# Kernel optimization log

Measured on AMD Instinct MI355X. Metric: run time of the kernel, lower is better.

## Reference

```python
import jax, jax.numpy as jnp
import numpy as np

D_MODEL, N_HEADS, N_KV, D_K = 4096, 32, 8, 128
N_REP = N_HEADS // N_KV  # n_kv_groups
SEQ = 2048
EPS = 1e-6


def _layernorm(x, gamma, beta):
    # LayerNorm over the last (d_k) axis
    mu = jnp.mean(x, axis=-1, keepdims=True)
    var = jnp.var(x, axis=-1, keepdims=True)
    return (x - mu) * jax.lax.rsqrt(var + EPS) * gamma + beta


def setup_inputs() -> dict:
    key = jax.random.key(0)
    ks = jax.random.split(key, 8)
    s = 0.02
    return {
        "x": jax.random.normal(ks[0], (1, SEQ, D_MODEL), jnp.float32),
        "k_cache": jnp.zeros((N_KV, SEQ, D_K), jnp.float32),
        "v_cache": jnp.zeros((N_KV, SEQ, D_K), jnp.float32),
        "Wq": jax.random.normal(ks[1], (N_HEADS * D_K, D_MODEL), jnp.float32) * s,
        "Wk": jax.random.normal(ks[2], (N_KV * D_K, D_MODEL), jnp.float32) * s,
        "Wv": jax.random.normal(ks[3], (N_KV * D_K, D_MODEL), jnp.float32) * s,
        "Wo": jax.random.normal(ks[4], (D_MODEL, D_MODEL), jnp.float32) * s,
        "q_gamma": jnp.ones((D_K,), jnp.float32),
        "q_beta": jnp.zeros((D_K,), jnp.float32),
        "k_gamma": jnp.ones((D_K,), jnp.float32),
        "k_beta": jnp.zeros((D_K,), jnp.float32),
        "positions": jnp.arange(SEQ, dtype=jnp.int32),
        "seq_id": 0,
    }


def reference(x, k_cache, v_cache, Wq, Wk, Wv, Wo, q_gamma, q_beta, k_gamma, k_beta, positions, seq_id):
    B, S, _ = x.shape
    # projections (no bias: attention_bias=False)
    q = (x @ Wq.T).reshape(B, S, N_HEADS, D_K)
    k = (x @ Wk.T).reshape(B, S, N_KV, D_K)
    v = (x @ Wv.T).reshape(B, S, N_KV, D_K)
    # per-head LayerNorm on d_k (q_norm / k_norm)
    q = _layernorm(q, q_gamma, q_beta)
    k = _layernorm(k, k_gamma, k_beta)
    # rotary in the source is identity (SimpleRotary returns x unchanged)
    # paged-cache update: scatter new K/V (batch 0) into cache at `positions`
    k_cache = k_cache.at[:, positions, :].set(jnp.swapaxes(k[0], 0, 1))  # [n_kv, S, d_k]
    v_cache = v_cache.at[:, positions, :].set(jnp.swapaxes(v[0], 0, 1))
    # gather cached KV up to max position (prefill: full SEQ, static for jit)
    K = k_cache[None, :, :S, :]  # [1, n_kv, S, d_k]
    V = v_cache[None, :, :S, :]
    # GQA repeat_kv: expand kv heads to n_heads
    K = jnp.repeat(K, N_REP, axis=1)  # [1, n_heads, S, d_k]
    V = jnp.repeat(V, N_REP, axis=1)
    Q = jnp.swapaxes(q, 1, 2)  # [B, n_heads, S, d_k]
    # causal SDPA (dropout_p=0 in eval)
    scores = jnp.einsum("bhqd,bhkd->bhqk", Q, K) / jnp.sqrt(jnp.float32(D_K))
    causal = jnp.tril(jnp.ones((S, S), dtype=bool))
    scores = jnp.where(causal, scores, jnp.finfo(scores.dtype).min)
    attn = jax.nn.softmax(scores, axis=-1)
    out = jnp.einsum("bhqk,bhkd->bhqd", attn, V)  # [B, n_heads, S, d_k]
    out = jnp.swapaxes(out, 1, 2).reshape(B, S, D_MODEL)
    return out @ Wo.T
```

## Files before the change

kernel.cpp:

```cpp
#include <hip/hip_runtime.h>
#include <stdint.h>

typedef short bf16x8 __attribute__((ext_vector_type(8)));
typedef float f32x4 __attribute__((ext_vector_type(4)));
typedef float f32x16 __attribute__((ext_vector_type(16)));

#define SEQ     2048
#define DM      4096
#define NQH     32
#define NKVH    8
#define DK      128
#define NQKV    6144

__device__ __forceinline__ unsigned short f2bfb(float f) {
    union { float f; unsigned u; } x; x.f = f;
    unsigned r = x.u + 0x7FFFu + ((x.u >> 16) & 1u);
    return (unsigned short)(r >> 16);
}

__device__ __forceinline__ unsigned cvt_pk_bf16(float a, float b) {
    unsigned r;
    asm("v_cvt_pk_bf16_f32 %0, %1, %2" : "=v"(r) : "v"(a), "v"(b));
    return r;
}

#if __has_builtin(__builtin_amdgcn_exp2f)
__device__ __forceinline__ float exp2_fast(float x) { return __builtin_amdgcn_exp2f(x); }
#else
__device__ __forceinline__ float exp2_fast(float x) { return exp2f(x); }
#endif

__device__ __forceinline__ void stage16(const void* g, void* l) {
    __builtin_amdgcn_global_load_lds(
        (const __attribute__((address_space(1))) void*)g,
        (__attribute__((address_space(3))) void*)l,
        16, 0, 0);
}

__global__ __launch_bounds__(256)
void cvt_bf16(const float4* __restrict__ src, ushort4* __restrict__ dst, int n4) {
    int i = blockIdx.x * 256 + threadIdx.x;
    const int stride = gridDim.x * 256;
    for (; i < n4; i += stride) {
        float4 f = src[i];
        ushort4 u;
        u.x = f2bfb(f.x); u.y = f2bfb(f.y); u.z = f2bfb(f.z); u.w = f2bfb(f.w);
        dst[i] = u;
    }
}

__global__ __launch_bounds__(256, 2)
void gemm_bt(const unsigned short* __restrict__ A, const unsigned short* __restrict__ B,
             float* __restrict__ C, int M, int N, int K)
{
    __shared__ __align__(16) unsigned short As[128 * 32];
    __shared__ __align__(16) unsigned short Bs[128 * 32];

    const int tid = threadIdx.x;
    const int w  = tid >> 6;
    const int l  = tid & 63;
    const int lr = l & 15;
    const int lg = l >> 4;
    const int m0 = blockIdx.y << 7;
    const int n0 = blockIdx.x << 7;
    const int wm = (w >> 1) << 6;
    const int wn = (w & 1) << 6;

    f32x4 acc[4][4];
#pragma unroll
    for (int i = 0; i < 4; ++i)
#pragma unroll
        for (int j = 0; j < 4; ++j) acc[i][j] = f32x4{0.f, 0.f, 0.f, 0.f};

    const int c0   = tid;
    const int row0 = c0 >> 2, kc0 = (c0 & 3) << 3;
    const int c1   = tid + 256;
    const int row1 = c1 >> 2, kc1 = (c1 & 3) << 3;
    const unsigned short* Ag = A + (size_t)m0 * K;
    const unsigned short* Bg = B + (size_t)n0 * K;
    char* AsB = (char*)As;
    char* BsB = (char*)Bs;
    const int wb = w << 10;

    const int nk = K >> 5;
    for (int kt = 0; kt < nk; ++kt) {
        const int ko = kt << 5;
        stage16(Ag + (size_t)row0 * K + ko + kc0, AsB + wb);
        stage16(Ag + (size_t)row1 * K + ko + kc1, AsB + 4096 + wb);
        stage16(Bg + (size_t)row0 * K + ko + kc0, BsB + wb);
        stage16(Bg + (size_t)row1 * K + ko + kc1, BsB + 4096 + wb);
        __syncthreads();

        bf16x8 af[4], bfr[4];
#pragma unroll
        for (int mi = 0; mi < 4; ++mi)
            af[mi] = *(const bf16x8*)(As + ((wm + (mi << 4) + lr) << 5) + (lg << 3));
#pragma unroll
        for (int ni = 0; ni < 4; ++ni)
            bfr[ni] = *(const bf16x8*)(Bs + ((wn + (ni << 4) + lr) << 5) + (lg << 3));
#pragma unroll
        for (int mi = 0; mi < 4; ++mi)
#pragma unroll
            for (int ni = 0; ni < 4; ++ni)
                acc[mi][ni] = __builtin_amdgcn_mfma_f32_16x16x32_bf16(af[mi], bfr[ni], acc[mi][ni], 0, 0, 0);
        __syncthreads();
    }

#pragma unroll
    for (int mi = 0; mi < 4; ++mi)
#pragma unroll
        for (int ni = 0; ni < 4; ++ni) {
            const int row = m0 + wm + (mi << 4) + (lg << 2);
            const int col = n0 + wn + (ni << 4) + lr;
            float* cp = C + (size_t)row * N + col;
#pragma unroll
            for (int r = 0; r < 4; ++r) cp[(size_t)r * N] = acc[mi][ni][r];
        }
}

__global__ __launch_bounds__(256)
void ln_qk(const float* __restrict__ Y,
           const float* __restrict__ qg, const float* __restrict__ qb,
           const float* __restrict__ kg, const float* __restrict__ kb,
           unsigned short* __restrict__ Q, unsigned short* __restrict__ Kc)
{
    const int seg = blockIdx.x * 4 + (threadIdx.x >> 6);
    const int l = threadIdx.x & 63;
    const int s = seg / 40;
    const int hh = seg - s * 40;

    const float* y = Y + (size_t)s * NQKV + hh * 128;
    float2 v = *(const float2*)(y + l * 2);
    float sum = v.x + v.y;
    float sq  = v.x * v.x + v.y * v.y;
#pragma unroll
    for (int d = 1; d < 64; d <<= 1) {
        sum += __shfl_xor(sum, d);
        sq  += __shfl_xor(sq, d);
    }
    const float mu  = sum * (1.f / 128.f);
    const float var = sq * (1.f / 128.f) - mu * mu;
    const float rs  = rsqrtf(var + 1e-6f);

    const float* g = (hh < 32) ? qg : kg;
    const float* b = (hh < 32) ? qb : kb;
    const float c = (hh < 32) ? (0.08838834764831845f * 1.4426950408889634f) : 1.0f;
    const float g0 = g[l * 2], g1 = g[l * 2 + 1];
    const float b0 = b[l * 2], b1 = b[l * 2 + 1];
    const unsigned short o0 = f2bfb(((v.x - mu) * rs * g0 + b0) * c);
    const unsigned short o1 = f2bfb(((v.y - mu) * rs * g1 + b1) * c);
    const unsigned pack = (unsigned)o0 | ((unsigned)o1 << 16);

    if (hh < 32) {
        unsigned* dst = (unsigned*)(Q + ((size_t)hh * SEQ + s) * 128 + l * 2);
        *dst = pack;
    } else {
        unsigned* dst = (unsigned*)(Kc + ((size_t)(hh - 32) * SEQ + s) * 128 + l * 2);
        *dst = pack;
    }
}

__global__ __launch_bounds__(256)
void v_transpose(const float* __restrict__ Y, unsigned short* __restrict__ Vt)
{
    __shared__ unsigned short t[64][132];
    const int h  = blockIdx.x;
    const int s0 = blockIdx.y << 6;
    const int tid = threadIdx.x;
    const float* y = Y + (size_t)s0 * NQKV + 5120 + h * 128;

#pragma unroll
    for (int p = 0; p < 16; ++p) {
        const int idx = p * 512 + tid * 2;
        const int s = idx >> 7, d = idx & 127;
        float2 v = *(const float2*)(y + (size_t)s * NQKV + d);
        t[s][d]     = f2bfb(v.x);
        t[s][d + 1] = f2bfb(v.y);
    }
    __syncthreads();
    unsigned short* out = Vt + (size_t)h * 128 * SEQ + s0;
#pragma unroll
    for (int p = 0; p < 16; ++p) {
        const int idx = p * 512 + tid * 2;
        const int d = idx >> 6, sp = idx & 63;
        unsigned pack = (unsigned)t[sp][d] | ((unsigned)t[sp + 1][d] << 16);
        *(unsigned*)(out + (size_t)d * SEQ + sp) = pack;
    }
}

__global__ __launch_bounds__(256, 2)
void attn(const unsigned short* __restrict__ Qb, const unsigned short* __restrict__ Kb,
          const unsigned short* __restrict__ Vt, unsigned short* __restrict__ Ob)
{
    __shared__ __align__(16) unsigned short Kl[2][64 * 128];
    __shared__ __align__(16) unsigned short Vl[2][128 * 64];

    const int h   = blockIdx.x;
    const int qt  = 15 - blockIdx.y;
    const int kvh = h >> 2;
    const int tid = threadIdx.x;
    const int w   = tid >> 6;
    const int l   = tid & 63;
    const int lq  = l & 31;
    const int hi  = l >> 5;
    const int q0  = qt << 7;
    const int wq  = q0 + (w << 5);
    const int qrow = wq + lq;

    const unsigned short* Qh = Qb + ((size_t)h * SEQ + wq) * 128;
    const unsigned short* Kh = Kb + (size_t)kvh * SEQ * 128;
    const unsigned short* Vh = Vt + (size_t)kvh * 128 * SEQ;

    int koff[4], voff[4];
#pragma unroll
    for (int p = 0; p < 4; ++p) {
        const int c  = p * 256 + tid;
        const int kr = c >> 4, kc = c & 15;
        koff[p] = kr * 128 + ((kc ^ (kr & 7)) << 3);
        const int vr = c >> 3, vc = c & 7;
        voff[p] = vr * SEQ + ((vc ^ (vr & 7)) << 3);
    }
    const int dstb = w << 10;

    bf16x8 qf[8];
#pragma unroll
    for (int ks = 0; ks < 8; ++ks)
        qf[ks] = *(const bf16x8*)(Qh + lq * 128 + ks * 16 + hi * 8);

    f32x16 o0_ = {0}, o1_ = {0}, o2_ = {0}, o3_ = {0};
    float m = -1.0e30f, lsum = 0.f;

    const int nt = (q0 + 128) >> 6;
    const int sw = (lq & 7) << 4;

#pragma unroll
    for (int p = 0; p < 4; ++p)
        stage16(Kh + koff[p], (char*)Kl[0] + p * 4096 + dstb);
#pragma unroll
    for (int p = 0; p < 4; ++p)
        stage16(Vh + voff[p], (char*)Vl[0] + p * 4096 + dstb);
    __syncthreads();

    int buf = 0;
    for (int t = 0; t < nt; ++t) {
        const int kv0 = t << 6;

        if (t + 1 < nt) {
            const int kvn = kv0 + 64;
#pragma unroll
            for (int p = 0; p < 4; ++p)
                stage16(Kh + (size_t)kvn * 128 + koff[p], (char*)(Kl[buf ^ 1]) + p * 4096 + dstb);
#pragma unroll
            for (int p = 0; p < 4; ++p)
                stage16(Vh + kvn + voff[p], (char*)(Vl[buf ^ 1]) + p * 4096 + dstb);
        }

        if (kv0 <= wq + 31) {
            const char* Kb0 = (const char*)(Kl[buf]) + lq * 256;
            const char* Kb1 = (const char*)(Kl[buf]) + (lq + 32) * 256;
            bf16x8 kf0[8], kf1[8];
#pragma unroll
            for (int ks = 0; ks < 8; ++ks) {
                const int cb = (ks * 32 + hi * 16) ^ sw;
                kf0[ks] = *(const bf16x8*)(Kb0 + cb);
                kf1[ks] = *(const bf16x8*)(Kb1 + cb);
            }
            f32x16 s0 = {0}, s1 = {0};
            __builtin_amdgcn_s_setprio(1);
#pragma unroll
            for (int ks = 0; ks < 8; ++ks) {
                s0 = __builtin_amdgcn_mfma_f32_32x32x16_bf16(kf0[ks], qf[ks], s0, 0, 0, 0);
                s1 = __builtin_amdgcn_mfma_f32_32x32x16_bf16(kf1[ks], qf[ks], s1, 0, 0, 0);
            }
            __builtin_amdgcn_s_setprio(0);

            if (kv0 + 63 > wq) {
#pragma unroll
                for (int r = 0; r < 16; ++r) {
                    const int kvl = (r & 3) + 8 * (r >> 2) + 4 * hi;
                    if (kv0 + kvl > qrow)      s0[r] = -1.0e30f;
                    if (kv0 + 32 + kvl > qrow) s1[r] = -1.0e30f;
                }
            }

            float m8[8];
#pragma unroll
            for (int i = 0; i < 8; ++i)
                m8[i] = fmaxf(fmaxf(s0[i], s0[i + 8]), fmaxf(s1[i], s1[i + 8]));
#pragma unroll
            for (int i = 0; i < 4; ++i) m8[i] = fmaxf(m8[i], m8[i + 4]);
            float pm = fmaxf(fmaxf(m8[0], m8[1]), fmaxf(m8[2], m8[3]));
            pm = fmaxf(pm, __shfl_xor(pm, 32));

            if (!__all(pm - m <= 8.0f)) {
                const float mn = fmaxf(m, pm);
                const float al = exp2_fast(m - mn);
                lsum *= al;
#pragma unroll
                for (int r = 0; r < 16; ++r) { o0_[r] *= al; o1_[r] *= al; o2_[r] *= al; o3_[r] *= al; }
                m = mn;
            }

#pragma unroll
            for (int r = 0; r < 16; ++r) s0[r] = exp2_fast(s0[r] - m);
#pragma unroll
            for (int r = 0; r < 16; ++r) s1[r] = exp2_fast(s1[r] - m);
            float a8[8];
#pragma unroll
            for (int i = 0; i < 8; ++i)
                a8[i] = (s0[i] + s0[i + 8]) + (s1[i] + s1[i + 8]);
#pragma unroll
            for (int i = 0; i < 4; ++i) a8[i] += a8[i + 4];
            float rs = (a8[0] + a8[1]) + (a8[2] + a8[3]);
            rs += __shfl_xor(rs, 32);
            lsum += rs;

            unsigned pw0[2][4], pw1[2][4];
#pragma unroll
            for (int u = 0; u < 4; ++u) {
                pw0[0][u] = cvt_pk_bf16(s0[u * 4 + 0], s0[u * 4 + 1]);
                pw1[0][u] = cvt_pk_bf16(s0[u * 4 + 2], s0[u * 4 + 3]);
                pw0[1][u] = cvt_pk_bf16(s1[u * 4 + 0], s1[u * 4 + 1]);
                pw1[1][u] = cvt_pk_bf16(s1[u * 4 + 2], s1[u * 4 + 3]);
            }

            const char* Vb = (const char*)(Vl[buf]);
#pragma unroll
            for (int ksg = 0; ksg < 4; ++ksg) {
                const int b  = ksg >> 1;
                const int ks = ksg & 1;
                const unsigned a0 = pw0[b][2 * ks],     a1 = pw1[b][2 * ks];
                const unsigned b0 = pw0[b][2 * ks + 1], b1 = pw1[b][2 * ks + 1];
                const unsigned sa0 = __shfl_xor(a0, 32);
                const unsigned sb0 = __shfl_xor(b0, 32);
                const unsigned sa1 = __shfl_xor(a1, 32);
                const unsigned sb1 = __shfl_xor(b1, 32);
                union { unsigned wrd[4]; bf16x8 v; } pb;
                pb.wrd[0] = hi ? sb0 : a0;
                pb.wrd[1] = hi ? sb1 : a1;
                pb.wrd[2] = hi ? b0  : sa0;
                pb.wrd[3] = hi ? b1  : sa1;

                const int cb = (ksg * 32 + hi * 16) ^ sw;
                bf16x8 vf0 = *(const bf16x8*)(Vb + (lq)       * 128 + cb);
                bf16x8 vf1 = *(const bf16x8*)(Vb + (lq + 32)  * 128 + cb);
                bf16x8 vf2 = *(const bf16x8*)(Vb + (lq + 64)  * 128 + cb);
                bf16x8 vf3 = *(const bf16x8*)(Vb + (lq + 96)  * 128 + cb);
                __builtin_amdgcn_s_setprio(1);
                o0_ = __builtin_amdgcn_mfma_f32_32x32x16_bf16(vf0, pb.v, o0_, 0, 0, 0);
                o1_ = __builtin_amdgcn_mfma_f32_32x32x16_bf16(vf1, pb.v, o1_, 0, 0, 0);
                o2_ = __builtin_amdgcn_mfma_f32_32x32x16_bf16(vf2, pb.v, o2_, 0, 0, 0);
                o3_ = __builtin_amdgcn_mfma_f32_32x32x16_bf16(vf3, pb.v, o3_, 0, 0, 0);
                __builtin_amdgcn_s_setprio(0);
            }
        }

        __syncthreads();
        buf ^= 1;
    }

    const float inv = 1.0f / lsum;
    unsigned short* orow = Ob + (size_t)qrow * DM + h * 128;
#pragma unroll
    for (int r = 0; r < 16; r += 2) {
        const int doff = 8 * (r >> 2) + 4 * hi + (r & 3);
        *(unsigned*)(orow + 0  + doff) = cvt_pk_bf16(o0_[r] * inv, o0_[r + 1] * inv);
        *(unsigned*)(orow + 32 + doff) = cvt_pk_bf16(o1_[r] * inv, o1_[r + 1] * inv);
        *(unsigned*)(orow + 64 + doff) = cvt_pk_bf16(o2_[r] * inv, o2_[r + 1] * inv);
        *(unsigned*)(orow + 96 + doff) = cvt_pk_bf16(o3_[r] * inv, o3_[r + 1] * inv);
    }
}

extern "C" void kernel_launch(void* const* d_in, const int* in_sizes, int n_in,
                              void* d_out, int out_size, void* d_ws, size_t ws_size,
                              hipStream_t stream)
{
    const float* x  = (const float*)d_in[0];
    const float* Wq = (const float*)d_in[3];
    const float* Wk = (const float*)d_in[4];
    const float* Wv = (const float*)d_in[5];
    const float* Wo = (const float*)d_in[6];
    const float* qg = (const float*)d_in[7];
    const float* qb = (const float*)d_in[8];
    const float* kg = (const float*)d_in[9];
    const float* kb = (const float*)d_in[10];
    float* out = (float*)d_out;

    char* ws = (char*)d_ws;
    unsigned short* xb   = (unsigned short*)(ws);
    unsigned short* wqkv = (unsigned short*)(ws + 16777216);
    unsigned short* wo   = (unsigned short*)(ws + 67108864);
    float*          y    = (float*)        (ws + 100663296);
    unsigned short* qbuf = (unsigned short*)(ws + 150994944);
    unsigned short* kbuf = (unsigned short*)(ws + 167772160);
    unsigned short* vtb  = (unsigned short*)(ws + 171966464);
    unsigned short* ob   = (unsigned short*)(ws + 176160768);

    {
        int n4 = (SEQ * DM) / 4;
        cvt_bf16<<<2048, 256, 0, stream>>>((const float4*)x, (ushort4*)xb, n4);
        n4 = (NQH * DK * DM) / 4;
        cvt_bf16<<<2048, 256, 0, stream>>>((const float4*)Wq, (ushort4*)wqkv, n4);
        n4 = (NKVH * DK * DM) / 4;
        cvt_bf16<<<2048, 256, 0, stream>>>((const float4*)Wk, (ushort4*)(wqkv + 16777216), n4);
        cvt_bf16<<<2048, 256, 0, stream>>>((const float4*)Wv, (ushort4*)(wqkv + 20971520), n4);
        n4 = (DM * DM) / 4;
        cvt_bf16<<<2048, 256, 0, stream>>>((const float4*)Wo, (ushort4*)wo, n4);
    }

    gemm_bt<<<dim3(NQKV / 128, SEQ / 128), 256, 0, stream>>>(xb, wqkv, y, SEQ, NQKV, DM);

    ln_qk<<<(SEQ * 40) / 4, 256, 0, stream>>>(y, qg, qb, kg, kb, qbuf, kbuf);

    v_transpose<<<dim3(NKVH, SEQ / 64), 256, 0, stream>>>(y, vtb);

    attn<<<dim3(NQH, SEQ / 128), 256, 0, stream>>>(qbuf, kbuf, vtb, ob);

    gemm_bt<<<dim3(DM / 128, SEQ / 128), 256, 0, stream>>>(ob, wo, out, SEQ, DM, DM);
}
```

Baseline: 527.9 us.

## Rewrite GEMM with 256x128 tiles, double-buffered LDS, XOR swizzle, block remap

Result: slower. 588.0 us (+11.4%).

```diff
diff --git a/kernel.cpp b/kernel.cpp
--- a/kernel.cpp
+++ b/kernel.cpp
@@ -49,69 +49,125 @@
     }
 }
 
-__global__ __launch_bounds__(256, 2)
-void gemm_bt(const unsigned short* __restrict__ A, const unsigned short* __restrict__ B,
+__global__ __launch_bounds__(512, 2)
+void gemm256(const unsigned short* __restrict__ A, const unsigned short* __restrict__ B,
              float* __restrict__ C, int M, int N, int K)
 {
-    __shared__ __align__(16) unsigned short As[128 * 32];
-    __shared__ __align__(16) unsigned short Bs[128 * 32];
+    __shared__ __align__(16) char lds[2 * 49152];
 
     const int tid = threadIdx.x;
-    const int w  = tid >> 6;
-    const int l  = tid & 63;
-    const int lr = l & 15;
-    const int lg = l >> 4;
-    const int m0 = blockIdx.y << 7;
-    const int n0 = blockIdx.x << 7;
-    const int wm = (w >> 1) << 6;
-    const int wn = (w & 1) << 6;
-
-    f32x4 acc[4][4];
-#pragma unroll
-    for (int i = 0; i < 4; ++i)
-#pragma unroll
-        for (int j = 0; j < 4; ++j) acc[i][j] = f32x4{0.f, 0.f, 0.f, 0.f};
-
-    const int c0   = tid;
-    const int row0 = c0 >> 2, kc0 = (c0 & 3) << 3;
-    const int c1   = tid + 256;
-    const int row1 = c1 >> 2, kc1 = (c1 & 3) << 3;
+    const int w   = tid >> 6;
+    const int l   = tid & 63;
+    const int lr  = l & 15;
+    const int lg  = l >> 4;
+    const int wr  = w >> 1;
+    const int wc  = w & 1;
+
+    const int nbn = N >> 7;
+    const int nwg = gridDim.x;
+    const int qz  = nwg >> 3;
+    const int id  = blockIdx.x;
+    const int swz = (id & 7) * qz + (id >> 3);
+    const int m0  = (swz / nbn) << 8;
+    const int n0  = (swz % nbn) << 7;
+
     const unsigned short* Ag = A + (size_t)m0 * K;
     const unsigned short* Bg = B + (size_t)n0 * K;
-    char* AsB = (char*)As;
-    char* BsB = (char*)Bs;
-    const int wb = w << 10;
-
-    const int nk = K >> 5;
-    for (int kt = 0; kt < nk; ++kt) {
-        const int ko = kt << 5;
-        stage16(Ag + (size_t)row0 * K + ko + kc0, AsB + wb);
-        stage16(Ag + (size_t)row1 * K + ko + kc1, AsB + 4096 + wb);
-        stage16(Bg + (size_t)row0 * K + ko + kc0, BsB + wb);
-        stage16(Bg + (size_t)row1 * K + ko + kc1, BsB + 4096 + wb);
-        __syncthreads();
-
-        bf16x8 af[4], bfr[4];
-#pragma unroll
-        for (int mi = 0; mi < 4; ++mi)
-            af[mi] = *(const bf16x8*)(As + ((wm + (mi << 4) + lr) << 5) + (lg << 3));
-#pragma unroll
-        for (int ni = 0; ni < 4; ++ni)
-            bfr[ni] = *(const bf16x8*)(Bs + ((wn + (ni << 4) + lr) << 5) + (lg << 3));
-#pragma unroll
-        for (int mi = 0; mi < 4; ++mi)
-#pragma unroll
-            for (int ni = 0; ni < 4; ++ni)
-                acc[mi][ni] = __builtin_amdgcn_mfma_f32_16x16x32_bf16(af[mi], bfr[ni], acc[mi][ni], 0, 0, 0);
-        __syncthreads();
-    }
+
+    int srow[6], scol[6];
+#pragma unroll
+    for (int u = 0; u < 6; ++u) {
+        const int p  = ((u < 4 ? u : u - 4) << 13) + tid * 16;
+        const int l2 = p ^ (((p >> 7) & 7) << 4);
+        srow[u] = l2 >> 7;
+        scol[u] = (l2 & 127) >> 1;
+    }
+
+    f32x4 acc[4][4];
+#pragma unroll
+    for (int i = 0; i < 4; ++i)
+#pragma unroll
+        for (int j = 0; j < 4; ++j) acc[i][j] = f32x4{0.f, 0.f, 0.f, 0.f};
+
+    const int NT = K >> 6;
+
+#define STAGE_TILE(kt, s)                                                            \
+    {                                                                                \
+        char* plane = lds + (s) * 49152;                                             \
+        const int k0 = (kt) << 6;                                                    \
+        _Pragma("unroll")                                                            \
+        for (int u = 0; u < 4; ++u)                                                  \
+            stage16(Ag + (size_t)srow[u] * K + k0 + scol[u],                         \
+                    plane + (u << 13) + tid * 16);                                   \
+        _Pragma("unroll")                                                            \
+        for (int u = 4; u < 6; ++u)                                                  \
+            stage16(Bg + (size_t)srow[u] * K + k0 + scol[u],                         \
+                    plane + 32768 + ((u - 4) << 13) + tid * 16);                     \
+    }
+
+    STAGE_TILE(0, 0)
+    asm volatile("s_waitcnt vmcnt(0)" ::: "memory");
+    __builtin_amdgcn_s_barrier();
+
+    for (int t = 0; t < NT; ++t) {
+        const int s = t & 1;
+        const char* pa = lds + s * 49152;
+        const char* pb = pa + 32768;
+
+#pragma unroll
+        for (int q = 0; q < 4; ++q) {
+            const int mi2 = q >> 1, ni2 = q & 1;
+
+            bf16x8 af[2][2], bfr[2][2];
+#pragma unroll
+            for (int mi = 0; mi < 2; ++mi) {
+                const int ra = wr * 64 + (mi2 * 2 + mi) * 16 + lr;
+                const int xo = (ra & 7) << 4;
+#pragma unroll
+                for (int ks = 0; ks < 2; ++ks)
+                    af[mi][ks] = *(const bf16x8*)(pa + ((ra * 128 + ks * 64 + lg * 16) ^ xo));
+            }
+#pragma unroll
+            for (int ni = 0; ni < 2; ++ni) {
+                const int rb = wc * 64 + (ni2 * 2 + ni) * 16 + lr;
+                const int xo = (rb & 7) << 4;
+#pragma unroll
+                for (int ks = 0; ks < 2; ++ks)
+                    bfr[ni][ks] = *(const bf16x8*)(pb + ((rb * 128 + ks * 64 + lg * 16) ^ xo));
+            }
+
+            if (q == 0 && t + 1 < NT) STAGE_TILE(t + 1, s ^ 1)
+
+            __builtin_amdgcn_s_barrier();
+            asm volatile("s_waitcnt lgkmcnt(0)" ::: "memory");
+            __builtin_amdgcn_sched_barrier(0);
+
+            __builtin_amdgcn_s_setprio(1);
+#pragma unroll
+            for (int mi = 0; mi < 2; ++mi)
+#pragma unroll
+                for (int ni = 0; ni < 2; ++ni)
+#pragma unroll
+                    for (int ks = 0; ks < 2; ++ks)
+                        acc[mi2 * 2 + mi][ni2 * 2 + ni] =
+                            __builtin_amdgcn_mfma_f32_16x16x32_bf16(
+                                af[mi][ks], bfr[ni][ks],
+                                acc[mi2 * 2 + mi][ni2 * 2 + ni], 0, 0, 0);
+            __builtin_amdgcn_s_setprio(0);
+
+            if (q == 3)
+                asm volatile("s_waitcnt vmcnt(0)" ::: "memory");
+            __builtin_amdgcn_s_barrier();
+        }
+    }
+#undef STAGE_TILE
 
 #pragma unroll
     for (int mi = 0; mi < 4; ++mi)
 #pragma unroll
         for (int ni = 0; ni < 4; ++ni) {
-            const int row = m0 + wm + (mi << 4) + (lg << 2);
-            const int col = n0 + wn + (ni << 4) + lr;
+            const int row = m0 + wr * 64 + mi * 16 + lg * 4;
+            const int col = n0 + wc * 64 + ni * 16 + lr;
             float* cp = C + (size_t)row * N + col;
 #pragma unroll
             for (int r = 0; r < 4; ++r) cp[(size_t)r * N] = acc[mi][ni][r];
@@ -408,7 +464,7 @@
         cvt_bf16<<<2048, 256, 0, stream>>>((const float4*)Wo, (ushort4*)wo, n4);
     }
 
-    gemm_bt<<<dim3(NQKV / 128, SEQ / 128), 256, 0, stream>>>(xb, wqkv, y, SEQ, NQKV, DM);
+    gemm256<<<(SEQ / 256) * (NQKV / 128), 512, 0, stream>>>(xb, wqkv, y, SEQ, NQKV, DM);
 
     ln_qk<<<(SEQ * 40) / 4, 256, 0, stream>>>(y, qg, qb, kg, kb, qbuf, kbuf);
 
@@ -416,5 +472,5 @@
 
     attn<<<dim3(NQH, SEQ / 128), 256, 0, stream>>>(qbuf, kbuf, vtb, ob);
 
-    gemm_bt<<<dim3(DM / 128, SEQ / 128), 256, 0, stream>>>(ob, wo, out, SEQ, DM, DM);
-}
+    gemm256<<<(SEQ / 256) * (DM / 128), 512, 0, stream>>>(ob, wo, out, SEQ, DM, DM);
+}
```

## Replace GEMM with 256x256-tile, 4-stage pipelined, swizzled LDS kernel

Applied to the files above, without the earlier changes.

Measured after the change: 531.5 us. About the same (+0.7%).

```diff
diff --git a/kernel.cpp b/kernel.cpp
--- a/kernel.cpp
+++ b/kernel.cpp
@@ -49,69 +49,103 @@
     }
 }
 
-__global__ __launch_bounds__(256, 2)
-void gemm_bt(const unsigned short* __restrict__ A, const unsigned short* __restrict__ B,
+__global__ __launch_bounds__(512, 1)
+void gemm_p4(const unsigned short* __restrict__ A, const unsigned short* __restrict__ B,
              float* __restrict__ C, int M, int N, int K)
 {
-    __shared__ __align__(16) unsigned short As[128 * 32];
-    __shared__ __align__(16) unsigned short Bs[128 * 32];
+    __shared__ __align__(16) char lds[4][32768];
 
     const int tid = threadIdx.x;
-    const int w  = tid >> 6;
-    const int l  = tid & 63;
-    const int lr = l & 15;
-    const int lg = l >> 4;
-    const int m0 = blockIdx.y << 7;
-    const int n0 = blockIdx.x << 7;
-    const int wm = (w >> 1) << 6;
-    const int wn = (w & 1) << 6;
-
-    f32x4 acc[4][4];
-#pragma unroll
-    for (int i = 0; i < 4; ++i)
-#pragma unroll
-        for (int j = 0; j < 4; ++j) acc[i][j] = f32x4{0.f, 0.f, 0.f, 0.f};
-
-    const int c0   = tid;
-    const int row0 = c0 >> 2, kc0 = (c0 & 3) << 3;
-    const int c1   = tid + 256;
-    const int row1 = c1 >> 2, kc1 = (c1 & 3) << 3;
+    const int w   = tid >> 6;
+    const int l   = tid & 63;
+    const int lr  = l & 15;
+    const int lg  = l >> 4;
+    const int wr  = w >> 2;
+    const int wc  = w & 3;
+
+    const int nbn = N >> 8;
+    const int qz  = gridDim.x >> 3;
+    const int id  = blockIdx.x;
+    const int swz = (id & 7) * qz + (id >> 3);
+    const int m0  = (swz / nbn) << 8;
+    const int n0  = (swz % nbn) << 8;
+
     const unsigned short* Ag = A + (size_t)m0 * K;
     const unsigned short* Bg = B + (size_t)n0 * K;
-    char* AsB = (char*)As;
-    char* BsB = (char*)Bs;
-    const int wb = w << 10;
-
-    const int nk = K >> 5;
-    for (int kt = 0; kt < nk; ++kt) {
-        const int ko = kt << 5;
-        stage16(Ag + (size_t)row0 * K + ko + kc0, AsB + wb);
-        stage16(Ag + (size_t)row1 * K + ko + kc1, AsB + 4096 + wb);
-        stage16(Bg + (size_t)row0 * K + ko + kc0, BsB + wb);
-        stage16(Bg + (size_t)row1 * K + ko + kc1, BsB + 4096 + wb);
-        __syncthreads();
-
-        bf16x8 af[4], bfr[4];
-#pragma unroll
-        for (int mi = 0; mi < 4; ++mi)
-            af[mi] = *(const bf16x8*)(As + ((wm + (mi << 4) + lr) << 5) + (lg << 3));
-#pragma unroll
-        for (int ni = 0; ni < 4; ++ni)
-            bfr[ni] = *(const bf16x8*)(Bs + ((wn + (ni << 4) + lr) << 5) + (lg << 3));
-#pragma unroll
-        for (int mi = 0; mi < 4; ++mi)
+
+    const int    srow  = tid >> 2;
+    const int    scs   = (tid & 3) ^ ((tid >> 3) & 3);
+    const size_t aoff0 = (size_t)srow * K + scs * 8;
+    const size_t aoff1 = (size_t)(srow + 128) * K + scs * 8;
+    const int    dsto  = tid * 16;
+
+    int offA[8], offB[4];
+#pragma unroll
+    for (int mi = 0; mi < 8; ++mi) {
+        const int row = wr * 128 + mi * 16 + lr;
+        offA[mi] = row * 64 + ((lg ^ ((row >> 1) & 3)) << 4);
+    }
+#pragma unroll
+    for (int ni = 0; ni < 4; ++ni) {
+        const int row = wc * 64 + ni * 16 + lr;
+        offB[ni] = 16384 + row * 64 + ((lg ^ ((row >> 1) & 3)) << 4);
+    }
+
+    f32x4 acc[8][4];
+#pragma unroll
+    for (int i = 0; i < 8; ++i)
+#pragma unroll
+        for (int j = 0; j < 4; ++j) acc[i][j] = f32x4{0.f, 0.f, 0.f, 0.f};
+
+    const int NT = K >> 5;
+
+#define STG(t)                                                   \
+    {                                                            \
+        char* pl = lds[(t) & 3];                                 \
+        const int k0 = (t) << 5;                                 \
+        stage16(Ag + aoff0 + k0, pl + dsto);                     \
+        stage16(Ag + aoff1 + k0, pl + 8192  + dsto);             \
+        stage16(Bg + aoff0 + k0, pl + 16384 + dsto);             \
+        stage16(Bg + aoff1 + k0, pl + 24576 + dsto);             \
+    }
+
+    STG(0) STG(1) STG(2)
+    asm volatile("s_waitcnt vmcnt(8)" ::: "memory");
+    __builtin_amdgcn_s_barrier();
+
+    for (int t = 0; t < NT; ++t) {
+        const char* pl = lds[t & 3];
+
+        bf16x8 af[8], bfv[4];
+#pragma unroll
+        for (int mi = 0; mi < 8; ++mi) af[mi] = *(const bf16x8*)(pl + offA[mi]);
+#pragma unroll
+        for (int ni = 0; ni < 4; ++ni) bfv[ni] = *(const bf16x8*)(pl + offB[ni]);
+
+        if (t + 3 < NT) STG(t + 3)
+
+        __builtin_amdgcn_s_setprio(1);
+#pragma unroll
+        for (int mi = 0; mi < 8; ++mi)
 #pragma unroll
             for (int ni = 0; ni < 4; ++ni)
-                acc[mi][ni] = __builtin_amdgcn_mfma_f32_16x16x32_bf16(af[mi], bfr[ni], acc[mi][ni], 0, 0, 0);
-        __syncthreads();
-    }
-
-#pragma unroll
-    for (int mi = 0; mi < 4; ++mi)
+                acc[mi][ni] = __builtin_amdgcn_mfma_f32_16x16x32_bf16(
+                    af[mi], bfv[ni], acc[mi][ni], 0, 0, 0);
+        __builtin_amdgcn_s_setprio(0);
+
+        if (t + 3 < NT)      { asm volatile("s_waitcnt vmcnt(8)" ::: "memory"); }
+        else if (t + 2 < NT) { asm volatile("s_waitcnt vmcnt(4)" ::: "memory"); }
+        else if (t + 1 < NT) { asm volatile("s_waitcnt vmcnt(0)" ::: "memory"); }
+        if (t + 1 < NT) __builtin_amdgcn_s_barrier();
+    }
+#undef STG
+
+#pragma unroll
+    for (int mi = 0; mi < 8; ++mi)
 #pragma unroll
         for (int ni = 0; ni < 4; ++ni) {
-            const int row = m0 + wm + (mi << 4) + (lg << 2);
-            const int col = n0 + wn + (ni << 4) + lr;
+            const int row = m0 + wr * 128 + mi * 16 + lg * 4;
+            const int col = n0 + wc * 64 + ni * 16 + lr;
             float* cp = C + (size_t)row * N + col;
 #pragma unroll
             for (int r = 0; r < 4; ++r) cp[(size_t)r * N] = acc[mi][ni][r];
@@ -408,7 +442,7 @@
         cvt_bf16<<<2048, 256, 0, stream>>>((const float4*)Wo, (ushort4*)wo, n4);
     }
 
-    gemm_bt<<<dim3(NQKV / 128, SEQ / 128), 256, 0, stream>>>(xb, wqkv, y, SEQ, NQKV, DM);
+    gemm_p4<<<(SEQ / 256) * (NQKV / 256), 512, 0, stream>>>(xb, wqkv, y, SEQ, NQKV, DM);
 
     ln_qk<<<(SEQ * 40) / 4, 256, 0, stream>>>(y, qg, qb, kg, kb, qbuf, kbuf);
 
@@ -416,5 +450,5 @@
 
     attn<<<dim3(NQH, SEQ / 128), 256, 0, stream>>>(qbuf, kbuf, vtb, ob);
 
-    gemm_bt<<<dim3(DM / 128, SEQ / 128), 256, 0, stream>>>(ob, wo, out, SEQ, DM, DM);
-}
+    gemm_p4<<<(SEQ / 256) * (DM / 256), 512, 0, stream>>>(ob, wo, out, SEQ, DM, DM);
+}
```
